# Performance work log

Measured on AMD Instinct MI355X. Metric: run time of the kernel, lower is better.

## Reference

```python
import jax, jax.numpy as jnp
import numpy as np

# ---- model hyperparams (match init_kwargs / Mamba1 defaults) ----
SEQ_LEN, PRED_LEN, PATCH, STRIDE = 512, 96, 16, 16
D_MODEL, N_LAYER, N_VARS = 128, 2, 32
D_INNER, D_STATE, D_CONV, DT_RANK = 2 * D_MODEL, 16, 4, 8  # d_inner=2*d_model, dt_rank=ceil(d_model/16)
BATCH = 16
EPS = 1e-5


def setup_inputs() -> dict:
    key = jax.random.key(0)
    ks = jax.random.split(key, 20)
    s = 0.02
    inp = {
        'x_enc': jax.random.normal(ks[0], (BATCH, SEQ_LEN, N_VARS), jnp.float32),
        'x_mark_enc': jax.random.normal(ks[1], (BATCH, SEQ_LEN, 4), jnp.float32),
        'x_dec': jax.random.normal(ks[2], (BATCH, PRED_LEN, N_VARS), jnp.float32),
        'x_mark_dec': jax.random.normal(ks[3], (BATCH, PRED_LEN, 4), jnp.float32),
        # patch embedding: Linear(patch_len -> d_model, bias=False)
        'patch_w': jax.random.normal(ks[4], (D_MODEL, PATCH), jnp.float32) * s,
        # per-layer Mamba1 params, stacked on leading layer axis
        'norm_w': jnp.ones((N_LAYER, D_MODEL), jnp.float32),
        'in_proj_w': jax.random.normal(ks[5], (N_LAYER, 2 * D_INNER, D_MODEL), jnp.float32) * s,
        'conv_w': jax.random.normal(ks[6], (N_LAYER, D_INNER, D_CONV), jnp.float32) * s,
        'conv_b': jnp.zeros((N_LAYER, D_INNER), jnp.float32),
        'x_proj_w': jax.random.normal(ks[7], (N_LAYER, DT_RANK + 2 * D_STATE, D_INNER), jnp.float32) * s,
        'dt_proj_w': jax.random.normal(ks[8], (N_LAYER, D_INNER, DT_RANK), jnp.float32) * s,
        'dt_proj_b': jax.random.normal(ks[9], (N_LAYER, D_INNER), jnp.float32) * 0.1 - 4.0,  # softplus -> small dt
        'A_log': jnp.tile(jnp.log(jnp.arange(1, D_STATE + 1, dtype=jnp.float32))[None, None, :], (N_LAYER, D_INNER, 1)),
        'D_skip': jnp.ones((N_LAYER, D_INNER), jnp.float32),
        'out_proj_w': jax.random.normal(ks[10], (N_LAYER, D_MODEL, D_INNER), jnp.float32) * s,
        'final_norm_w': jnp.ones((D_MODEL,), jnp.float32),
        # head: Linear(d_model*seq_len//patch_len -> pred_len)
        'head_w': jax.random.normal(ks[11], (PRED_LEN, D_MODEL * SEQ_LEN // PATCH), jnp.float32) * s,
        'head_b': jnp.zeros((PRED_LEN,), jnp.float32),
    }
    return inp


def rmsnorm(x, w):
    return x * jax.lax.rsqrt(jnp.mean(x * x, axis=-1, keepdims=True) + EPS) * w


def selective_scan(u, dt, A, Bm, Cm, Dp):
    # u, dt: (B,L,Di); Bm, Cm: (B,L,N); A: (Di,N); Dp: (Di,)
    def step(h, inp):
        dt_t, B_t, C_t, u_t = inp  # (B,Di),(B,N),(B,N),(B,Di)
        dA = jnp.exp(dt_t[:, :, None] * A)                      # (B,Di,N)
        h = dA * h + dt_t[:, :, None] * B_t[:, None, :] * u_t[:, :, None]
        y = jnp.einsum('bdn,bn->bd', h, C_t)
        return h, y

    B_, L, Di = u.shape
    h0 = jnp.zeros((B_, Di, A.shape[1]), u.dtype)
    xs = (dt.transpose(1, 0, 2), Bm.transpose(1, 0, 2), Cm.transpose(1, 0, 2), u.transpose(1, 0, 2))
    _, ys = jax.lax.scan(step, h0, xs)
    return ys.transpose(1, 0, 2) + u * Dp  # skip connection D*u


def mamba_mixer(x, in_w, cw, cb, xp_w, dt_w, dt_b, A_log, Dp, out_w):
    # x: (B,L,d_model)
    xz = x @ in_w.T                                   # (B,L,2*Di)
    xs_, z = jnp.split(xz, 2, axis=-1)
    xc = xs_.transpose(0, 2, 1)                       # (B,Di,L)
    xc = jax.lax.conv_general_dilated(
        xc, cw[:, None, :], (1,), [(D_CONV - 1, 0)],  # causal depthwise conv
        dimension_numbers=('NCH', 'OIH', 'NCH'), feature_group_count=D_INNER)
    xc = jax.nn.silu(xc + cb[None, :, None])
    u = xc.transpose(0, 2, 1)                         # (B,L,Di)
    x_dbl = u @ xp_w.T                                # (B,L,dt_rank+2N)
    dt, Bm, Cm = jnp.split(x_dbl, [DT_RANK, DT_RANK + D_STATE], axis=-1)
    dt = jax.nn.softplus(dt @ dt_w.T + dt_b)          # (B,L,Di)
    A = -jnp.exp(A_log)                               # (Di,N)
    y = selective_scan(u, dt, A, Bm, Cm, Dp)
    y = y * jax.nn.silu(z)
    return y @ out_w.T


def reference(x_enc, x_mark_enc, x_dec, x_mark_dec, patch_w, norm_w, in_proj_w,
              conv_w, conv_b, x_proj_w, dt_proj_w, dt_proj_b, A_log, D_skip,
              out_proj_w, final_norm_w, head_w, head_b):
    b, _, c = x_enc.shape
    # instance norm over time (stats detached)
    means = jax.lax.stop_gradient(jnp.mean(x_enc, axis=1, keepdims=True))
    xe = x_enc - means
    stdev = jax.lax.stop_gradient(jnp.sqrt(jnp.var(xe, axis=1, keepdims=True) + EPS))
    xe = xe / stdev
    # patching: stride == patch_len so unfold == reshape
    xp = xe.transpose(0, 2, 1).reshape(b, c, SEQ_LEN // PATCH, PATCH)  # (b,c,l,patch)
    enc = jnp.einsum('bclp,dp->bcld', xp, patch_w).reshape(b, c * (SEQ_LEN // PATCH), D_MODEL)
    # Mamba encoder: pre-norm residual blocks + final norm
    x = enc
    for i in range(N_LAYER):
        h = rmsnorm(x, norm_w[i])
        x = x + mamba_mixer(h, in_proj_w[i], conv_w[i], conv_b[i], x_proj_w[i],
                            dt_proj_w[i], dt_proj_b[i], A_log[i], D_skip[i], out_proj_w[i])
    x = rmsnorm(x, final_norm_w)
    # prediction head: b (c l) d -> (b c) (l d) -> linear -> (b, pred, c)
    l = SEQ_LEN // PATCH
    xh = x.reshape(b, c, l * D_MODEL)
    out = xh @ head_w.T + head_b                      # (b,c,pred)
    dec_out = out.transpose(0, 2, 1)                  # (b,pred,c)
    dec_out = dec_out * stdev[:, :1, :] + means[:, :1, :]
    return dec_out
```

## Files before the change

kernel.cpp:

```cpp
#include <hip/hip_runtime.h>
#include <hip/hip_bf16.h>
#include <math.h>

#define BATCH   16
#define SEQL    512
#define NVARS   32
#define PATCHL  16
#define LTOK    32
#define DMODEL  128
#define NLAYER  2
#define DIN     256
#define DSTATE  16
#define DTRANK  8
#define DCONV   4
#define PRED    96
#define TOK     1024
#define NTOK    (BATCH*TOK)
#define EPSF    1e-5f
#define NCH     64
#define CHL     16

#define NIW (NLAYER * 2 * DIN * DMODEL)
#define NXW (NLAYER * (DTRANK + 2*DSTATE) * DIN)
#define NOW (NLAYER * DMODEL * DIN)
#define NHW (PRED * LTOK * DMODEL)
#define TOTW (NIW + NXW + NOW + NHW)

typedef __attribute__((ext_vector_type(8))) short bf16x8;
typedef __attribute__((ext_vector_type(4))) float f32x4;
typedef __hip_bfloat16 bf16;

__device__ __forceinline__ float softplus_f(float x) {
    return (x > 8.f) ? x : __logf(1.f + __expf(x));
}

__global__ __launch_bounds__(256) void k_init(
    const float* __restrict__ x_enc, const float* __restrict__ patch_w,
    const float* __restrict__ nw0,
    const float* __restrict__ in_w, const float* __restrict__ xp_w,
    const float* __restrict__ out_w, const float* __restrict__ head_w,
    const float* __restrict__ A_log,
    float* __restrict__ x, bf16* __restrict__ hbf,
    float* __restrict__ means, float* __restrict__ stdev,
    bf16* __restrict__ wbf, float* __restrict__ a1s, int* __restrict__ pwf,
    float* __restrict__ hg)
{
    __shared__ float xe[SEQL];
    __shared__ float pw[DMODEL * PATCHL];
    __shared__ float red[8];
    __shared__ float enc_lds[LTOK][DMODEL];
    int tid = threadIdx.x;

    if (blockIdx.x >= BATCH * NVARS) {
        int i = (blockIdx.x - BATCH * NVARS) * 256 + tid;
        if (i < TOTW) {
            float v;
            if (i < NIW) v = in_w[i];
            else if (i < NIW + NXW) v = xp_w[i - NIW];
            else if (i < NIW + NXW + NOW) v = out_w[i - NIW - NXW];
            else v = head_w[i - NIW - NXW - NOW];
            wbf[i] = __float2bfloat16(v);
        } else if (i < TOTW + NLAYER * DIN) {
            int j = i - TOTW;
            const float* al = A_log + (size_t)j * DSTATE;
            float a1 = -__expf(al[0]);
            bool pwok = true;
            #pragma unroll
            for (int n = 1; n < 16; n++) {
                float av = -__expf(al[n]);
                pwok = pwok && (fabsf(av - (n + 1) * a1) <= 1e-5f * fabsf((n + 1) * a1));
            }
            a1s[j] = a1;
            pwf[j] = pwok ? 1 : 0;
        } else if (i < TOTW + NLAYER * DIN + 512 * PRED) {
            hg[i - TOTW - NLAYER * DIN] = 0.f;
        }
        return;
    }

    int bc = blockIdx.x;
    int b = bc >> 5, c = bc & 31;

    float v0 = x_enc[((size_t)b * SEQL + tid) * NVARS + c];
    float v1 = x_enc[((size_t)b * SEQL + tid + 256) * NVARS + c];
    for (int i = tid; i < DMODEL * PATCHL; i += 256) pw[i] = patch_w[i];

    float s = v0 + v1;
    for (int o = 1; o < 64; o <<= 1) s += __shfl_xor(s, o, 64);
    if ((tid & 63) == 0) red[tid >> 6] = s;
    __syncthreads();
    float mean = (red[0] + red[1] + red[2] + red[3]) * (1.f / 512.f);

    float d0 = v0 - mean, d1 = v1 - mean;
    float q = d0 * d0 + d1 * d1;
    for (int o = 1; o < 64; o <<= 1) q += __shfl_xor(q, o, 64);
    if ((tid & 63) == 0) red[4 + (tid >> 6)] = q;
    __syncthreads();
    float var = (red[4] + red[5] + red[6] + red[7]) * (1.f / 512.f);
    float sd = sqrtf(var + EPSF);
    float rsd = 1.f / sd;
    if (tid == 0) { means[bc] = mean; stdev[bc] = sd; }

    xe[tid] = d0 * rsd;
    xe[tid + 256] = d1 * rsd;
    __syncthreads();

    size_t base = ((size_t)b * TOK + (size_t)c * LTOK) * DMODEL;
    for (int o = tid; o < LTOK * DMODEL; o += 256) {
        int l = o >> 7, dm = o & 127;
        float acc = 0.f;
        #pragma unroll
        for (int p = 0; p < PATCHL; p++) acc += xe[l * PATCHL + p] * pw[dm * PATCHL + p];
        x[base + o] = acc;
        enc_lds[l][dm] = acc;
    }
    __syncthreads();

    int t = tid >> 3, g = tid & 7;
    float vals[16];
    float ss = 0.f;
    #pragma unroll
    for (int j = 0; j < 16; j++) { vals[j] = enc_lds[t][g * 16 + j]; ss += vals[j] * vals[j]; }
    ss += __shfl_xor(ss, 1, 64);
    ss += __shfl_xor(ss, 2, 64);
    ss += __shfl_xor(ss, 4, 64);
    float rms = rsqrtf(ss * (1.f / DMODEL) + EPSF);
    bf16* hp = hbf + (base + (size_t)t * DMODEL);
    #pragma unroll
    for (int j = 0; j < 16; j++)
        hp[g * 16 + j] = __float2bfloat16(vals[j] * rms * nw0[g * 16 + j]);
}

__global__ __launch_bounds__(256) void mfma_gemm_at(
    const bf16* __restrict__ A, const bf16* __restrict__ W,
    float* __restrict__ C, int M, int N, int K, int kper)
{
    __shared__ ushort Asm[128][40];
    __shared__ ushort Wsm[128][40];
    int bm = blockIdx.y * 128, bn = blockIdx.x * 128;
    int tid = threadIdx.x;
    int w = tid >> 6, l = tid & 63;
    int wr = w >> 1, wc = w & 1;
    int kb = (l >> 4) * 8, lr = l & 15;

    f32x4 acc[4][4];
    #pragma unroll
    for (int i = 0; i < 4; i++)
        #pragma unroll
        for (int j = 0; j < 4; j++) acc[i][j] = (f32x4){0.f, 0.f, 0.f, 0.f};

    int kbeg = blockIdx.z * kper;
    for (int k0 = kbeg; k0 < kbeg + kper; k0 += 32) {
        #pragma unroll
        for (int i = 0; i < 2; i++) {
            int idx = tid + 256 * i;
            int row = idx >> 2, kq = (idx & 3) * 8;
            *(float4*)&Asm[row][kq] =
                *(const float4*)&A[(size_t)(bm + row) * K + k0 + kq];
            float4 wv = make_float4(0.f, 0.f, 0.f, 0.f);
            if (bn + row < N)
                wv = *(const float4*)&W[(size_t)(bn + row) * K + k0 + kq];
            *(float4*)&Wsm[row][kq] = wv;
        }
        __syncthreads();
        bf16x8 af[4], bfr[4];
        #pragma unroll
        for (int f = 0; f < 4; f++) {
            af[f]  = *(const bf16x8*)&Asm[wr * 64 + f * 16 + lr][kb];
            bfr[f] = *(const bf16x8*)&Wsm[wc * 64 + f * 16 + lr][kb];
        }
        #pragma unroll
        for (int mf = 0; mf < 4; mf++)
            #pragma unroll
            for (int nf = 0; nf < 4; nf++)
                acc[mf][nf] = __builtin_amdgcn_mfma_f32_16x16x32_bf16(
                    af[mf], bfr[nf], acc[mf][nf], 0, 0, 0);
        __syncthreads();
    }

    int rbase = bm + wr * 64 + (l >> 4) * 4;
    int cbase = bn + wc * 64 + lr;
    #pragma unroll
    for (int mf = 0; mf < 4; mf++) {
        #pragma unroll
        for (int nf = 0; nf < 4; nf++) {
            int n = cbase + nf * 16;
            if (n >= N) continue;
            #pragma unroll
            for (int r = 0; r < 4; r++)
                atomicAdd(&C[(size_t)(rbase + mf * 16 + r) * N + n], acc[mf][nf][r]);
        }
    }
}

__global__ __launch_bounds__(256) void k_convx1(
    const bf16* __restrict__ hbf, const bf16* __restrict__ iwA,
    const float* __restrict__ cw, const float* __restrict__ cb,
    const bf16* __restrict__ xw,
    const float* __restrict__ dtw, const float* __restrict__ dtb_,
    const float* __restrict__ a1s, const int* __restrict__ pwf,
    const float* __restrict__ A_log,
    unsigned int* __restrict__ udb, float* __restrict__ xdbl,
    bf16* __restrict__ q, float* __restrict__ sdt_out)
{
    int blk = blockIdx.x;
    int b = blk >> 6, ch = blk & (NCH - 1);
    int d = threadIdx.x;
    __shared__ __align__(16) char smem[25600];
    ushort (*hb_lds)[136] = (ushort(*)[136])smem;
    ushort (*xs_lds)[264] = (ushort(*)[264])(smem + 8704);
    ushort (*u_lds)[264]  = (ushort(*)[264])smem;
    float  (*xdbl_lds)[40] = (float(*)[40])(smem + 8704);

    int tloc0 = ch * CHL;

    {
        int r = d >> 3, c8 = (d & 7) * 16;
        int tl = tloc0 - 16 + r;
        float4 v0 = make_float4(0.f, 0.f, 0.f, 0.f), v1 = v0;
        if (tl >= 0) {
            const bf16* src = hbf + ((size_t)b * TOK + tl) * DMODEL + c8;
            v0 = *(const float4*)src;
            v1 = *(const float4*)(src + 8);
        }
        *(float4*)&hb_lds[r][c8] = v0;
        *(float4*)&hb_lds[r][c8 + 8] = v1;
    }
    __syncthreads();

    {
        int w = d >> 6, l = d & 63;
        int lr = l & 15, kb = (l >> 4) * 8;
        f32x4 accx[2][4];
        #pragma unroll
        for (int mf = 0; mf < 2; mf++)
            #pragma unroll
            for (int nf = 0; nf < 4; nf++) accx[mf][nf] = (f32x4){0.f, 0.f, 0.f, 0.f};
        #pragma unroll
        for (int ks = 0; ks < 4; ks++) {
            bf16x8 af0 = *(const bf16x8*)&hb_lds[lr][ks * 32 + kb];
            bf16x8 af1 = *(const bf16x8*)&hb_lds[16 + lr][ks * 32 + kb];
            #pragma unroll
            for (int nf = 0; nf < 4; nf++) {
                const bf16* wrow = iwA + (size_t)(w * 64 + nf * 16 + lr) * DMODEL;
                bf16x8 bfr = *(const bf16x8*)&wrow[ks * 32 + kb];
                accx[0][nf] = __builtin_amdgcn_mfma_f32_16x16x32_bf16(af0, bfr, accx[0][nf], 0, 0, 0);
                accx[1][nf] = __builtin_amdgcn_mfma_f32_16x16x32_bf16(af1, bfr, accx[1][nf], 0, 0, 0);
            }
        }
        __syncthreads();
        #pragma unroll
        for (int mf = 0; mf < 2; mf++)
            #pragma unroll
            for (int nf = 0; nf < 4; nf++) {
                int ncol = w * 64 + nf * 16 + lr;
                #pragma unroll
                for (int r = 0; r < 4; r++) {
                    int row = mf * 16 + (l >> 4) * 4 + r;
                    bf16 xb = __float2bfloat16(accx[mf][nf][r]);
                    xs_lds[row][ncol] = *(ushort*)&xb;
                }
            }
    }
    __syncthreads();

    {
        float c0 = cw[d * 4], c1 = cw[d * 4 + 1], c2 = cw[d * 4 + 2], c3 = cw[d * 4 + 3];
        float cbias = cb[d];
        float xv[19];
        #pragma unroll
        for (int i = 0; i < 19; i++) {
            ushort raw = xs_lds[13 + i][d];
            xv[i] = __bfloat162float(*(bf16*)&raw);
        }
        #pragma unroll
        for (int t = 0; t < 16; t++) {
            float a = cbias + xv[t] * c0 + xv[t + 1] * c1 + xv[t + 2] * c2 + xv[t + 3] * c3;
            float s = __fdividef(a, 1.f + __expf(-a));
            bf16 ub = __float2bfloat16(s);
            u_lds[t][d] = *(ushort*)&ub;
        }
    }
    __syncthreads();

    {
        int w = d >> 6, l = d & 63;
        if (w < 3) {
            int lr = l & 15, kb = (l >> 4) * 8;
            int nrow = w * 16 + lr;
            bool valid = nrow < 40;
            const bf16* wrow = xw + (size_t)nrow * 256;
            f32x4 acc = (f32x4){0.f, 0.f, 0.f, 0.f};
            #pragma unroll
            for (int ks = 0; ks < 8; ks++) {
                bf16x8 af = *(const bf16x8*)&u_lds[lr][ks * 32 + kb];
                bf16x8 bfr = (bf16x8){0, 0, 0, 0, 0, 0, 0, 0};
                if (valid) bfr = *(const bf16x8*)&wrow[ks * 32 + kb];
                acc = __builtin_amdgcn_mfma_f32_16x16x32_bf16(af, bfr, acc, 0, 0, 0);
            }
            int ncol = w * 16 + (l & 15);
            if (ncol < 40) {
                #pragma unroll
                for (int r = 0; r < 4; r++) {
                    int t = (l >> 4) * 4 + r;
                    xdbl_lds[t][ncol] = acc[r];
                    xdbl[((size_t)b * TOK + tloc0 + t) * 40 + ncol] = acc[r];
                }
            }
        }
    }
    __syncthreads();

    float a1 = a1s[d];
    bool pw = pwf[d] != 0;
    float w8[8];
    #pragma unroll
    for (int j = 0; j < 8; j++) w8[j] = dtw[d * 8 + j];
    float bias = dtb_[d];
    float h[16];
    #pragma unroll
    for (int n = 0; n < 16; n++) h[n] = 0.f;
    float sdt = 0.f;
    unsigned int* udp = udb + ((size_t)b * TOK + tloc0) * 256 + d;

    if (pw) {
        for (int t = 0; t < CHL; t++) {
            float acc = bias;
            #pragma unroll
            for (int j = 0; j < 8; j++) acc += xdbl_lds[t][j] * w8[j];
            float dtv = softplus_f(acc);
            ushort uraw = u_lds[t][d];
            float uu = __bfloat162float(*(bf16*)&uraw);
            sdt += dtv;
            float du = dtv * uu;
            float dA[16];
            dA[0] = __expf(dtv * a1);
            #pragma unroll
            for (int n = 1; n < 16; n++) dA[n] = dA[(n - 1) >> 1] * dA[n >> 1];
            #pragma unroll
            for (int n = 0; n < 16; n++)
                h[n] = dA[n] * h[n] + du * xdbl_lds[t][8 + n];
            bf16 dv = __float2bfloat16(dtv);
            udp[(size_t)t * 256] = (unsigned int)uraw | ((unsigned int)(*(ushort*)&dv) << 16);
        }
    } else {
        float Av[16];
        #pragma unroll
        for (int n = 0; n < 16; n++) Av[n] = -__expf(A_log[d * 16 + n]);
        for (int t = 0; t < CHL; t++) {
            float acc = bias;
            #pragma unroll
            for (int j = 0; j < 8; j++) acc += xdbl_lds[t][j] * w8[j];
            float dtv = softplus_f(acc);
            ushort uraw = u_lds[t][d];
            float uu = __bfloat162float(*(bf16*)&uraw);
            sdt += dtv;
            float du = dtv * uu;
            #pragma unroll
            for (int n = 0; n < 16; n++)
                h[n] = __expf(dtv * Av[n]) * h[n] + du * xdbl_lds[t][8 + n];
            bf16 dv = __float2bfloat16(dtv);
            udp[(size_t)t * 256] = (unsigned int)uraw | ((unsigned int)(*(ushort*)&dv) << 16);
        }
    }
    bf16* qp = q + ((size_t)blk * 16) * 256 + d;
    #pragma unroll
    for (int n = 0; n < 16; n++) qp[(size_t)n * 256] = __float2bfloat16(h[n]);
    sdt_out[(size_t)blk * 256 + d] = sdt;
}

__global__ __launch_bounds__(256) void k_scan2(
    const float* __restrict__ A_log, const float* __restrict__ sdt_in,
    bf16* __restrict__ q)
{
    int idx = blockIdx.x * 256 + threadIdx.x;
    int d = idx & 255, n = (idx >> 8) & 15, b = idx >> 12;
    float Av = -__expf(A_log[d * 16 + n]);
    float h = 0.f;
    for (int g = 0; g < NCH / 8; g++) {
        float qv[8], sv[8];
        #pragma unroll
        for (int j = 0; j < 8; j++) {
            size_t blk = (size_t)b * NCH + g * 8 + j;
            qv[j] = __bfloat162float(q[(blk * 16 + n) * 256 + d]);
            sv[j] = sdt_in[blk * 256 + d];
        }
        #pragma unroll
        for (int j = 0; j < 8; j++) {
            size_t blk = (size_t)b * NCH + g * 8 + j;
            float P = __expf(Av * sv[j]);
            q[(blk * 16 + n) * 256 + d] = __float2bfloat16(h);
            h = P * h + qv[j];
        }
    }
}

__global__ __launch_bounds__(256) void k_scan3o(
    const unsigned int* __restrict__ udb, const float* __restrict__ xdbl,
    const bf16* __restrict__ iwZ,
    const float* __restrict__ a1s, const int* __restrict__ pwf,
    const float* __restrict__ A_log, const float* __restrict__ Dp,
    const bf16* __restrict__ q, const bf16* __restrict__ ow,
    const float* __restrict__ nwn,
    float* __restrict__ x, bf16* __restrict__ hbf)
{
    int blk = blockIdx.x;
    int b = blk >> 6, ch = blk & (NCH - 1);
    int d = threadIdx.x;
    __shared__ __align__(16) char smem[21248];
    ushort (*hz_lds)[136] = (ushort(*)[136])smem;
    ushort (*z_lds)[264]  = (ushort(*)[264])(smem + 4352);
    ushort (*y_lds)[264]  = (ushort(*)[264])(smem + 12800);
    float  (*xn_lds)[132] = (float(*)[132])smem;

    size_t tok0 = (size_t)b * TOK + ch * CHL;

    {
        int r = d >> 4, c8 = (d & 15) * 8;
        *(float4*)&hz_lds[r][c8] = *(const float4*)(hbf + (tok0 + r) * DMODEL + c8);
    }
    __syncthreads();

    {
        int w = d >> 6, l = d & 63;
        int lr = l & 15, kb = (l >> 4) * 8;
        f32x4 accz[4];
        #pragma unroll
        for (int nf = 0; nf < 4; nf++) accz[nf] = (f32x4){0.f, 0.f, 0.f, 0.f};
        #pragma unroll
        for (int ks = 0; ks < 4; ks++) {
            bf16x8 af = *(const bf16x8*)&hz_lds[lr][ks * 32 + kb];
            #pragma unroll
            for (int nf = 0; nf < 4; nf++) {
                const bf16* wrow = iwZ + (size_t)(w * 64 + nf * 16 + lr) * DMODEL;
                bf16x8 bfr = *(const bf16x8*)&wrow[ks * 32 + kb];
                accz[nf] = __builtin_amdgcn_mfma_f32_16x16x32_bf16(af, bfr, accz[nf], 0, 0, 0);
            }
        }
        #pragma unroll
        for (int nf = 0; nf < 4; nf++) {
            int ncol = w * 64 + nf * 16 + lr;
            #pragma unroll
            for (int r = 0; r < 4; r++) {
                bf16 zb = __float2bfloat16(accz[nf][r]);
                z_lds[(l >> 4) * 4 + r][ncol] = *(ushort*)&zb;
            }
        }
    }
    __syncthreads();

    float a1 = a1s[d];
    bool pw = pwf[d] != 0;
    float Dv = Dp[d];
    float h[16];
    const bf16* qp = q + ((size_t)blk * 16) * 256 + d;
    #pragma unroll
    for (int n = 0; n < 16; n++) h[n] = __bfloat162float(qp[(size_t)n * 256]);

    const float* row = xdbl + tok0 * 40;
    const unsigned int* up = udb + tok0 * 256 + d;

    if (pw) {
        for (int t = 0; t < CHL; t++, row += 40, up += 256) {
            unsigned int ud = *up;
            ushort ulo = (ushort)(ud & 0xffffu), dhi = (ushort)(ud >> 16);
            float uu = __bfloat162float(*(bf16*)&ulo);
            float dtv = __bfloat162float(*(bf16*)&dhi);
            float du = dtv * uu;
            float dA[16];
            dA[0] = __expf(dtv * a1);
            #pragma unroll
            for (int n = 1; n < 16; n++) dA[n] = dA[(n - 1) >> 1] * dA[n >> 1];
            float ya = 0.f;
            #pragma unroll
            for (int n = 0; n < 16; n++) {
                h[n] = dA[n] * h[n] + du * row[8 + n];
                ya += h[n] * row[24 + n];
            }
            ushort zraw = z_lds[t][d];
            float zv = __bfloat162float(*(bf16*)&zraw);
            float sz = __fdividef(zv, 1.f + __expf(-zv));
            bf16 yb = __float2bfloat16((ya + uu * Dv) * sz);
            y_lds[t][d] = *(ushort*)&yb;
        }
    } else {
        float Av[16];
        #pragma unroll
        for (int n = 0; n < 16; n++) Av[n] = -__expf(A_log[d * 16 + n]);
        for (int t = 0; t < CHL; t++, row += 40, up += 256) {
            unsigned int ud = *up;
            ushort ulo = (ushort)(ud & 0xffffu), dhi = (ushort)(ud >> 16);
            float uu = __bfloat162float(*(bf16*)&ulo);
            float dtv = __bfloat162float(*(bf16*)&dhi);
            float du = dtv * uu;
            float ya = 0.f;
            #pragma unroll
            for (int n = 0; n < 16; n++) {
                h[n] = __expf(dtv * Av[n]) * h[n] + du * row[8 + n];
                ya += h[n] * row[24 + n];
            }
            ushort zraw = z_lds[t][d];
            float zv = __bfloat162float(*(bf16*)&zraw);
            float sz = __fdividef(zv, 1.f + __expf(-zv));
            bf16 yb = __float2bfloat16((ya + uu * Dv) * sz);
            y_lds[t][d] = *(ushort*)&yb;
        }
    }
    __syncthreads();

    int w = d >> 6, l = d & 63;
    int lr = l & 15, kb = (l >> 4) * 8;
    const bf16* wr0 = ow + (size_t)(w * 32 + lr) * 256;
    const bf16* wr1 = ow + (size_t)(w * 32 + 16 + lr) * 256;
    f32x4 acc0 = (f32x4){0.f, 0.f, 0.f, 0.f};
    f32x4 acc1 = (f32x4){0.f, 0.f, 0.f, 0.f};
    #pragma unroll
    for (int ks = 0; ks < 8; ks++) {
        bf16x8 af = *(const bf16x8*)&y_lds[lr][ks * 32 + kb];
        bf16x8 b0 = *(const bf16x8*)&wr0[ks * 32 + kb];
        bf16x8 b1 = *(const bf16x8*)&wr1[ks * 32 + kb];
        acc0 = __builtin_amdgcn_mfma_f32_16x16x32_bf16(af, b0, acc0, 0, 0, 0);
        acc1 = __builtin_amdgcn_mfma_f32_16x16x32_bf16(af, b1, acc1, 0, 0, 0);
    }
    int trow = (l >> 4) * 4;
    float* xp = x + (tok0 + trow) * (size_t)DMODEL;
    #pragma unroll
    for (int r = 0; r < 4; r++) {
        float v0 = xp[(size_t)r * DMODEL + w * 32 + lr] + acc0[r];
        float v1 = xp[(size_t)r * DMODEL + w * 32 + 16 + lr] + acc1[r];
        xp[(size_t)r * DMODEL + w * 32 + lr] = v0;
        xp[(size_t)r * DMODEL + w * 32 + 16 + lr] = v1;
        xn_lds[trow + r][w * 32 + lr] = v0;
        xn_lds[trow + r][w * 32 + 16 + lr] = v1;
    }
    __syncthreads();

    {
        int t = d >> 4, g = d & 15;
        float vals[8];
        float ss = 0.f;
        #pragma unroll
        for (int j = 0; j < 8; j++) { vals[j] = xn_lds[t][g * 8 + j]; ss += vals[j] * vals[j]; }
        ss += __shfl_xor(ss, 1, 64);
        ss += __shfl_xor(ss, 2, 64);
        ss += __shfl_xor(ss, 4, 64);
        ss += __shfl_xor(ss, 8, 64);
        float rms = rsqrtf(ss * (1.f / DMODEL) + EPSF);
        bf16* hp = hbf + (tok0 + t) * (size_t)DMODEL;
        #pragma unroll
        for (int j = 0; j < 8; j++)
            hp[g * 8 + j] = __float2bfloat16(vals[j] * rms * nwn[g * 8 + j]);
    }
}

__global__ __launch_bounds__(256) void k_head_ep(
    const float* __restrict__ hg, const float* __restrict__ hb,
    const float* __restrict__ means, const float* __restrict__ stdev,
    float* __restrict__ out)
{
    int i = blockIdx.x * 256 + threadIdx.x;
    if (i >= BATCH * PRED * NVARS) return;
    int c = i & 31;
    int p = (i >> 5) % PRED;
    int b = i / (PRED * NVARS);
    float v = hg[((size_t)b * NVARS + c) * PRED + p] + hb[p];
    out[i] = v * stdev[b * NVARS + c] + means[b * NVARS + c];
}

extern "C" void kernel_launch(void* const* d_in, const int* in_sizes, int n_in,
                              void* d_out, int out_size, void* d_ws, size_t ws_size,
                              hipStream_t stream)
{
    const float* x_enc   = (const float*)d_in[0];
    const float* patch_w = (const float*)d_in[4];
    const float* norm_w  = (const float*)d_in[5];
    const float* in_w    = (const float*)d_in[6];
    const float* conv_w  = (const float*)d_in[7];
    const float* conv_b  = (const float*)d_in[8];
    const float* xp_w    = (const float*)d_in[9];
    const float* dt_w    = (const float*)d_in[10];
    const float* dt_b    = (const float*)d_in[11];
    const float* A_log   = (const float*)d_in[12];
    const float* D_skip  = (const float*)d_in[13];
    const float* out_w   = (const float*)d_in[14];
    const float* fnorm_w = (const float*)d_in[15];
    const float* head_w  = (const float*)d_in[16];
    const float* head_b  = (const float*)d_in[17];
    float* out = (float*)d_out;

    float* ws    = (float*)d_ws;
    float* means = ws;
    float* stdv  = ws + 512;
    float* x     = ws + 1024;
    float* xdbl  = x    + (size_t)NTOK * 128;
    float* sbuf  = xdbl + (size_t)NTOK * 40;
    float* hg    = sbuf + (size_t)BATCH * NCH * DIN;
    float* a1s   = hg + 512 * PRED;
    int*   pwf   = (int*)(a1s + NLAYER * DIN);
    unsigned int* udb = (unsigned int*)(pwf + NLAYER * DIN);
    bf16* hbf  = (bf16*)(udb + (size_t)NTOK * 256);
    bf16* qbuf = hbf + (size_t)NTOK * 128;
    bf16* wbf  = qbuf + (size_t)BATCH * NCH * DSTATE * DIN;

    bf16* iwbf = wbf;
    bf16* xwbf = iwbf + NIW;
    bf16* owbf = xwbf + NXW;
    bf16* hwbf = owbf + NOW;

    int castN = TOTW + NLAYER * DIN + 512 * PRED;
    int initBlocks = BATCH * NVARS + (castN + 255) / 256;
    k_init<<<initBlocks, 256, 0, stream>>>(
        x_enc, patch_w, norm_w, in_w, xp_w, out_w, head_w, A_log,
        x, hbf, means, stdv, wbf, a1s, pwf, hg);

    for (int layer = 0; layer < NLAYER; layer++) {
        const float* cw  = conv_w + layer * DIN * DCONV;
        const float* cb  = conv_b + layer * DIN;
        const float* dw  = dt_w   + layer * DIN * DTRANK;
        const float* db  = dt_b   + layer * DIN;
        const float* al  = A_log  + layer * DIN * DSTATE;
        const float* dp  = D_skip + layer * DIN;
        const float* a1l = a1s + layer * DIN;
        const int*   pwl = pwf + layer * DIN;
        const bf16* iwA = iwbf + (size_t)layer * 2 * DIN * DMODEL;
        const bf16* iwZ = iwA + (size_t)DIN * DMODEL;
        const bf16* xw = xwbf + (size_t)layer * (DTRANK + 2 * DSTATE) * DIN;
        const bf16* ow = owbf + (size_t)layer * DMODEL * DIN;
        const float* nwn = (layer + 1 < NLAYER) ? (norm_w + (layer + 1) * DMODEL) : fnorm_w;

        k_convx1<<<BATCH * NCH, 256, 0, stream>>>(
            hbf, iwA, cw, cb, xw, dw, db, a1l, pwl, al, udb, xdbl, qbuf, sbuf);
        k_scan2<<<(BATCH * DIN * DSTATE) / 256, 256, 0, stream>>>(al, sbuf, qbuf);
        k_scan3o<<<BATCH * NCH, 256, 0, stream>>>(
            udb, xdbl, iwZ, a1l, pwl, al, dp, qbuf, ow, nwn, x, hbf);
    }

    mfma_gemm_at<<<dim3(1, 4, 32), 256, 0, stream>>>(
        hbf, hwbf, hg, 512, PRED, LTOK * DMODEL, 128);
    k_head_ep<<<(BATCH * PRED * NVARS + 255) / 256, 256, 0, stream>>>(
        hg, head_b, means, stdv, out);
}
```

Measured before the change: 147.1 us.

## Move z projection GEMM into conv kernel and pass z via packed buffer

Computes the z half of in_proj inside k_convx1, reusing the hidden-state tile already in shared memory. The z values are stored next to u/dt in a widened uint2 per-token buffer, so k_scan3o no longer reloads hbf or runs its own z GEMM. The aim is to remove that duplicated load and MFMA stage and one barrier from the scan-output kernel. In exchange the intermediate buffer doubles in size and half of the added word is unused, which raises global memory traffic. The larger buffer also shifts the workspace layout.

```diff
diff --git a/kernel.cpp b/kernel.cpp
--- a/kernel.cpp
+++ b/kernel.cpp
@@ -195,12 +195,13 @@
 
 __global__ __launch_bounds__(256) void k_convx1(
     const bf16* __restrict__ hbf, const bf16* __restrict__ iwA,
+    const bf16* __restrict__ iwZ,
     const float* __restrict__ cw, const float* __restrict__ cb,
     const bf16* __restrict__ xw,
     const float* __restrict__ dtw, const float* __restrict__ dtb_,
     const float* __restrict__ a1s, const int* __restrict__ pwf,
     const float* __restrict__ A_log,
-    unsigned int* __restrict__ udb, float* __restrict__ xdbl,
+    uint2* __restrict__ udb, float* __restrict__ xdbl,
     bf16* __restrict__ q, float* __restrict__ sdt_out)
 {
     int blk = blockIdx.x;
@@ -210,7 +211,8 @@
     ushort (*hb_lds)[136] = (ushort(*)[136])smem;
     ushort (*xs_lds)[264] = (ushort(*)[264])(smem + 8704);
     ushort (*u_lds)[264]  = (ushort(*)[264])smem;
-    float  (*xdbl_lds)[40] = (float(*)[40])(smem + 8704);
+    ushort (*z_lds)[264]  = (ushort(*)[264])(smem + 8704);
+    float  (*xdbl_lds)[40] = (float(*)[40])(smem + 17152);
 
     int tloc0 = ch * CHL;
 
@@ -228,9 +230,12 @@
     }
     __syncthreads();
 
+    int w = d >> 6, l = d & 63;
+    int lr = l & 15, kb = (l >> 4) * 8;
+    f32x4 accz[4];
+    #pragma unroll
+    for (int nf = 0; nf < 4; nf++) accz[nf] = (f32x4){0.f, 0.f, 0.f, 0.f};
     {
-        int w = d >> 6, l = d & 63;
-        int lr = l & 15, kb = (l >> 4) * 8;
         f32x4 accx[2][4];
         #pragma unroll
         for (int mf = 0; mf < 2; mf++)
@@ -242,10 +247,13 @@
             bf16x8 af1 = *(const bf16x8*)&hb_lds[16 + lr][ks * 32 + kb];
             #pragma unroll
             for (int nf = 0; nf < 4; nf++) {
-                const bf16* wrow = iwA + (size_t)(w * 64 + nf * 16 + lr) * DMODEL;
-                bf16x8 bfr = *(const bf16x8*)&wrow[ks * 32 + kb];
-                accx[0][nf] = __builtin_amdgcn_mfma_f32_16x16x32_bf16(af0, bfr, accx[0][nf], 0, 0, 0);
-                accx[1][nf] = __builtin_amdgcn_mfma_f32_16x16x32_bf16(af1, bfr, accx[1][nf], 0, 0, 0);
+                const bf16* wrowA = iwA + (size_t)(w * 64 + nf * 16 + lr) * DMODEL;
+                const bf16* wrowZ = iwZ + (size_t)(w * 64 + nf * 16 + lr) * DMODEL;
+                bf16x8 bA = *(const bf16x8*)&wrowA[ks * 32 + kb];
+                bf16x8 bZ = *(const bf16x8*)&wrowZ[ks * 32 + kb];
+                accx[0][nf] = __builtin_amdgcn_mfma_f32_16x16x32_bf16(af0, bA, accx[0][nf], 0, 0, 0);
+                accx[1][nf] = __builtin_amdgcn_mfma_f32_16x16x32_bf16(af1, bA, accx[1][nf], 0, 0, 0);
+                accz[nf]    = __builtin_amdgcn_mfma_f32_16x16x32_bf16(af1, bZ, accz[nf],    0, 0, 0);
             }
         }
         __syncthreads();
@@ -284,9 +292,16 @@
     __syncthreads();
 
     {
-        int w = d >> 6, l = d & 63;
+        #pragma unroll
+        for (int nf = 0; nf < 4; nf++) {
+            int ncol = w * 64 + nf * 16 + lr;
+            #pragma unroll
+            for (int r = 0; r < 4; r++) {
+                bf16 zb = __float2bfloat16(accz[nf][r]);
+                z_lds[(l >> 4) * 4 + r][ncol] = *(ushort*)&zb;
+            }
+        }
         if (w < 3) {
-            int lr = l & 15, kb = (l >> 4) * 8;
             int nrow = w * 16 + lr;
             bool valid = nrow < 40;
             const bf16* wrow = xw + (size_t)nrow * 256;
@@ -321,7 +336,7 @@
     #pragma unroll
     for (int n = 0; n < 16; n++) h[n] = 0.f;
     float sdt = 0.f;
-    unsigned int* udp = udb + ((size_t)b * TOK + tloc0) * 256 + d;
+    uint2* udp = udb + ((size_t)b * TOK + tloc0) * 256 + d;
 
     if (pw) {
         for (int t = 0; t < CHL; t++) {
@@ -330,6 +345,7 @@
             for (int j = 0; j < 8; j++) acc += xdbl_lds[t][j] * w8[j];
             float dtv = softplus_f(acc);
             ushort uraw = u_lds[t][d];
+            ushort zraw = z_lds[t][d];
             float uu = __bfloat162float(*(bf16*)&uraw);
             sdt += dtv;
             float du = dtv * uu;
@@ -341,7 +357,9 @@
             for (int n = 0; n < 16; n++)
                 h[n] = dA[n] * h[n] + du * xdbl_lds[t][8 + n];
             bf16 dv = __float2bfloat16(dtv);
-            udp[(size_t)t * 256] = (unsigned int)uraw | ((unsigned int)(*(ushort*)&dv) << 16);
+            udp[(size_t)t * 256] = make_uint2(
+                (unsigned int)uraw | ((unsigned int)(*(ushort*)&dv) << 16),
+                (unsigned int)zraw);
         }
     } else {
         float Av[16];
@@ -353,6 +371,7 @@
             for (int j = 0; j < 8; j++) acc += xdbl_lds[t][j] * w8[j];
             float dtv = softplus_f(acc);
             ushort uraw = u_lds[t][d];
+            ushort zraw = z_lds[t][d];
             float uu = __bfloat162float(*(bf16*)&uraw);
             sdt += dtv;
             float du = dtv * uu;
@@ -360,7 +379,9 @@
             for (int n = 0; n < 16; n++)
                 h[n] = __expf(dtv * Av[n]) * h[n] + du * xdbl_lds[t][8 + n];
             bf16 dv = __float2bfloat16(dtv);
-            udp[(size_t)t * 256] = (unsigned int)uraw | ((unsigned int)(*(ushort*)&dv) << 16);
+            udp[(size_t)t * 256] = make_uint2(
+                (unsigned int)uraw | ((unsigned int)(*(ushort*)&dv) << 16),
+                (unsigned int)zraw);
         }
     }
     bf16* qp = q + ((size_t)blk * 16) * 256 + d;
@@ -396,8 +417,7 @@
 }
 
 __global__ __launch_bounds__(256) void k_scan3o(
-    const unsigned int* __restrict__ udb, const float* __restrict__ xdbl,
-    const bf16* __restrict__ iwZ,
+    const uint2* __restrict__ udb, const float* __restrict__ xdbl,
     const float* __restrict__ a1s, const int* __restrict__ pwf,
     const float* __restrict__ A_log, const float* __restrict__ Dp,
     const bf16* __restrict__ q, const bf16* __restrict__ ow,
@@ -407,47 +427,10 @@
     int blk = blockIdx.x;
     int b = blk >> 6, ch = blk & (NCH - 1);
     int d = threadIdx.x;
-    __shared__ __align__(16) char smem[21248];
-    ushort (*hz_lds)[136] = (ushort(*)[136])smem;
-    ushort (*z_lds)[264]  = (ushort(*)[264])(smem + 4352);
-    ushort (*y_lds)[264]  = (ushort(*)[264])(smem + 12800);
-    float  (*xn_lds)[132] = (float(*)[132])smem;
+    __shared__ ushort y_lds[16][264];
+    __shared__ float xn_lds[16][132];
 
     size_t tok0 = (size_t)b * TOK + ch * CHL;
-
-    {
-        int r = d >> 4, c8 = (d & 15) * 8;
-        *(float4*)&hz_lds[r][c8] = *(const float4*)(hbf + (tok0 + r) * DMODEL + c8);
-    }
-    __syncthreads();
-
-    {
-        int w = d >> 6, l = d & 63;
-        int lr = l & 15, kb = (l >> 4) * 8;
-        f32x4 accz[4];
-        #pragma unroll
-        for (int nf = 0; nf < 4; nf++) accz[nf] = (f32x4){0.f, 0.f, 0.f, 0.f};
-        #pragma unroll
-        for (int ks = 0; ks < 4; ks++) {
-            bf16x8 af = *(const bf16x8*)&hz_lds[lr][ks * 32 + kb];
-            #pragma unroll
-            for (int nf = 0; nf < 4; nf++) {
-                const bf16* wrow = iwZ + (size_t)(w * 64 + nf * 16 + lr) * DMODEL;
-                bf16x8 bfr = *(const bf16x8*)&wrow[ks * 32 + kb];
-                accz[nf] = __builtin_amdgcn_mfma_f32_16x16x32_bf16(af, bfr, accz[nf], 0, 0, 0);
-            }
-        }
-        #pragma unroll
-        for (int nf = 0; nf < 4; nf++) {
-            int ncol = w * 64 + nf * 16 + lr;
-            #pragma unroll
-            for (int r = 0; r < 4; r++) {
-                bf16 zb = __float2bfloat16(accz[nf][r]);
-                z_lds[(l >> 4) * 4 + r][ncol] = *(ushort*)&zb;
-            }
-        }
-    }
-    __syncthreads();
 
     float a1 = a1s[d];
     bool pw = pwf[d] != 0;
@@ -458,12 +441,13 @@
     for (int n = 0; n < 16; n++) h[n] = __bfloat162float(qp[(size_t)n * 256]);
 
     const float* row = xdbl + tok0 * 40;
-    const unsigned int* up = udb + tok0 * 256 + d;
+    const uint2* up = udb + tok0 * 256 + d;
 
     if (pw) {
         for (int t = 0; t < CHL; t++, row += 40, up += 256) {
-            unsigned int ud = *up;
-            ushort ulo = (ushort)(ud & 0xffffu), dhi = (ushort)(ud >> 16);
+            uint2 ud = *up;
+            ushort ulo = (ushort)(ud.x & 0xffffu), dhi = (ushort)(ud.x >> 16);
+            ushort zraw = (ushort)(ud.y & 0xffffu);
             float uu = __bfloat162float(*(bf16*)&ulo);
             float dtv = __bfloat162float(*(bf16*)&dhi);
             float du = dtv * uu;
@@ -477,7 +461,6 @@
                 h[n] = dA[n] * h[n] + du * row[8 + n];
                 ya += h[n] * row[24 + n];
             }
-            ushort zraw = z_lds[t][d];
             float zv = __bfloat162float(*(bf16*)&zraw);
             float sz = __fdividef(zv, 1.f + __expf(-zv));
             bf16 yb = __float2bfloat16((ya + uu * Dv) * sz);
@@ -488,8 +471,9 @@
         #pragma unroll
         for (int n = 0; n < 16; n++) Av[n] = -__expf(A_log[d * 16 + n]);
         for (int t = 0; t < CHL; t++, row += 40, up += 256) {
-            unsigned int ud = *up;
-            ushort ulo = (ushort)(ud & 0xffffu), dhi = (ushort)(ud >> 16);
+            uint2 ud = *up;
+            ushort ulo = (ushort)(ud.x & 0xffffu), dhi = (ushort)(ud.x >> 16);
+            ushort zraw = (ushort)(ud.y & 0xffffu);
             float uu = __bfloat162float(*(bf16*)&ulo);
             float dtv = __bfloat162float(*(bf16*)&dhi);
             float du = dtv * uu;
@@ -499,7 +483,6 @@
                 h[n] = __expf(dtv * Av[n]) * h[n] + du * row[8 + n];
                 ya += h[n] * row[24 + n];
             }
-            ushort zraw = z_lds[t][d];
             float zv = __bfloat162float(*(bf16*)&zraw);
             float sz = __fdividef(zv, 1.f + __expf(-zv));
             bf16 yb = __float2bfloat16((ya + uu * Dv) * sz);
@@ -597,7 +580,7 @@
     float* hg    = sbuf + (size_t)BATCH * NCH * DIN;
     float* a1s   = hg + 512 * PRED;
     int*   pwf   = (int*)(a1s + NLAYER * DIN);
-    unsigned int* udb = (unsigned int*)(pwf + NLAYER * DIN);
+    uint2* udb   = (uint2*)(pwf + NLAYER * DIN);
     bf16* hbf  = (bf16*)(udb + (size_t)NTOK * 256);
     bf16* qbuf = hbf + (size_t)NTOK * 128;
     bf16* wbf  = qbuf + (size_t)BATCH * NCH * DSTATE * DIN;
@@ -629,10 +612,10 @@
         const float* nwn = (layer + 1 < NLAYER) ? (norm_w + (layer + 1) * DMODEL) : fnorm_w;
 
         k_convx1<<<BATCH * NCH, 256, 0, stream>>>(
-            hbf, iwA, cw, cb, xw, dw, db, a1l, pwl, al, udb, xdbl, qbuf, sbuf);
+            hbf, iwA, iwZ, cw, cb, xw, dw, db, a1l, pwl, al, udb, xdbl, qbuf, sbuf);
         k_scan2<<<(BATCH * DIN * DSTATE) / 256, 256, 0, stream>>>(al, sbuf, qbuf);
         k_scan3o<<<BATCH * NCH, 256, 0, stream>>>(
-            udb, xdbl, iwZ, a1l, pwl, al, dp, qbuf, ow, nwn, x, hbf);
+            udb, xdbl, a1l, pwl, al, dp, qbuf, ow, nwn, x, hbf);
     }
 
     mfma_gemm_at<<<dim3(1, 4, 32), 256, 0, stream>>>(
```

After: 160.1 us. 8.8% more time.
